# Performance work log

Hardware: AMD Instinct MI355X
Metric: run time of the kernel (lower is better)

## Reference

```python
import jax, jax.numpy as jnp
import numpy as np

GCN_DIM, GEO_DIM, HIDDEN_DIM, TOWER_DIM, RECENT_K = 128, 32, 256, 128, 50
NUM_ITEMS, NUM_USERS = 100000, 16384


def _normalize(x, eps=1e-12):
    # torch F.normalize(dim=1): x / max(||x||, eps)
    n = jnp.linalg.norm(x, axis=1, keepdims=True)
    return x / jnp.maximum(n, eps)


def setup_inputs() -> dict:
    key = jax.random.key(0)
    ks = jax.random.split(key, 16)
    s = 0.05  # weight init scale
    return {
        "item_feat": jax.random.normal(ks[0], (NUM_ITEMS, 2), jnp.float32),
        "gcn_item_emb": jax.random.normal(ks[1], (NUM_ITEMS, GCN_DIM), jnp.float32),
        "gcn_user_emb": jax.random.normal(ks[2], (NUM_USERS, GCN_DIM), jnp.float32),
        "user_items": jax.random.randint(ks[3], (NUM_USERS, RECENT_K), 0, NUM_ITEMS, jnp.int32),
        "Wg": s * jax.random.normal(ks[4], (2, GEO_DIM), jnp.float32),
        "bg": jnp.zeros((GEO_DIM,), jnp.float32),
        "Wi1": s * jax.random.normal(ks[5], (GCN_DIM + GEO_DIM, HIDDEN_DIM), jnp.float32),
        "bi1": jnp.zeros((HIDDEN_DIM,), jnp.float32),
        "Wi2": s * jax.random.normal(ks[6], (HIDDEN_DIM, TOWER_DIM), jnp.float32),
        "bi2": jnp.zeros((TOWER_DIM,), jnp.float32),
        "Wq": s * jax.random.normal(ks[7], (GCN_DIM, TOWER_DIM), jnp.float32),
        "bq": jnp.zeros((TOWER_DIM,), jnp.float32),
        "Wk": s * jax.random.normal(ks[8], (TOWER_DIM, TOWER_DIM), jnp.float32),
        "bk": jnp.zeros((TOWER_DIM,), jnp.float32),
        "Wu1": s * jax.random.normal(ks[9], (GCN_DIM + TOWER_DIM, HIDDEN_DIM), jnp.float32),
        "bu1": jnp.zeros((HIDDEN_DIM,), jnp.float32),
        "Wu2": s * jax.random.normal(ks[10], (HIDDEN_DIM, TOWER_DIM), jnp.float32),
        "bu2": jnp.zeros((TOWER_DIM,), jnp.float32),
    }


def reference(item_feat, gcn_item_emb, gcn_user_emb, user_items,
              Wg, bg, Wi1, bi1, Wi2, bi2, Wq, bq, Wk, bk, Wu1, bu1, Wu2, bu2):
    # ---- encode_items ----
    geo = jax.nn.relu(item_feat @ Wg + bg)                       # [I, GEO]
    xi = jnp.concatenate([geo, gcn_item_emb], axis=1)            # [I, GEO+GCN]
    item_emb = _normalize(jax.nn.relu(xi @ Wi1 + bi1) @ Wi2 + bi2)  # [I, T]

    # ---- encode_users (batched ragged attention pooling) ----
    h = item_emb[user_items]                                     # [U, K, T] gather
    q = gcn_user_emb @ Wq + bq                                   # [U, T]
    k = h @ Wk + bk                                              # [U, K, T]
    scores = jnp.einsum('ut,ukt->uk', q, k)                      # [U, K]
    alpha = jax.nn.softmax(scores, axis=1)                       # softmax over history
    rep = jnp.einsum('uk,ukt->ut', alpha, h)                     # [U, T]
    fused = jnp.concatenate([gcn_user_emb, rep], axis=1)         # [U, GCN+T]
    user_emb = _normalize(jax.nn.relu(fused @ Wu1 + bu1) @ Wu2 + bu2)  # [U, T]

    return jnp.concatenate([item_emb, user_emb], axis=0)         # [I+U, T]
```

## Files before the change

### kernel.cpp

```cpp
#include <hip/hip_runtime.h>
#include <hip/hip_bf16.h>
#include <math.h>

#define NITEMS 100000
#define NUSERS 16384
#define GCN 128
#define GEO 32
#define HIDD 256
#define TD 128
#define RK 50

typedef unsigned int uint;
typedef unsigned short ushort;
typedef __bf16 bf16x8 __attribute__((ext_vector_type(8)));
typedef float f32x4 __attribute__((ext_vector_type(4)));

__device__ __forceinline__ ushort bfb(float x) {
  union { __hip_bfloat16 b; ushort u; } t; t.b = __float2bfloat16(x); return t.u;
}
__device__ __forceinline__ uint packbf2(float a, float b) {
  return (uint)bfb(a) | ((uint)bfb(b) << 16);
}
__device__ __forceinline__ float bflo(uint d) { return __uint_as_float(d << 16); }
__device__ __forceinline__ float bfhi(uint d) { return __uint_as_float(d & 0xffff0000u); }

union U4B { uint4 u; bf16x8 b; };
__device__ __forceinline__ bf16x8 ldfrag(const ushort* p) { U4B t; t.u = *(const uint4*)p; return t.b; }

__global__ __launch_bounds__(256) void prep_convert(
    const float* __restrict__ Wi1, const float* __restrict__ Wi2,
    const float* __restrict__ Wu1, const float* __restrict__ Wu2,
    ushort* __restrict__ Wi1P, ushort* __restrict__ Wi2P,
    ushort* __restrict__ Wu1P, ushort* __restrict__ Wu2P)
{
  int id = blockIdx.x * 256 + threadIdx.x;
  if (id < 40960) {
    int k = id >> 8, c = id & 255;
    Wi1P[(k >> 5) * 8192 + c * 32 + (k & 31)] = bfb(Wi1[id]);
  } else if (id < 73728) {
    int i = id - 40960; int k = i >> 7, c = i & 127;
    Wi2P[(k >> 5) * 4096 + c * 32 + (k & 31)] = bfb(Wi2[i]);
  } else if (id < 139264) {
    int i = id - 73728; int k = i >> 8, c = i & 255;
    Wu1P[(k >> 5) * 8192 + c * 32 + (k & 31)] = bfb(Wu1[i]);
  } else if (id < 172032) {
    int i = id - 139264; int k = i >> 7, c = i & 127;
    Wu2P[(k >> 5) * 4096 + c * 32 + (k & 31)] = bfb(Wu2[i]);
  }
}

__global__ __launch_bounds__(256) void prep_wqk(
    const float* __restrict__ Wq, const float* __restrict__ Wk,
    const float* __restrict__ bq, float* __restrict__ WqkS, float* __restrict__ bqk)
{
  int id = blockIdx.x * 256 + threadIdx.x;
  if (id < 16384) {
    int g = id >> 7, s = id & 127;
    float acc = 0.f;
    for (int t = 0; t < 128; t += 4) {
      float4 a = *(const float4*)(Wq + g * 128 + t);
      float4 b = *(const float4*)(Wk + s * 128 + t);
      acc += a.x * b.x + a.y * b.y + a.z * b.z + a.w * b.w;
    }
    WqkS[g * 128 + s] = acc;
  } else if (id < 16512) {
    int s = id - 16384;
    float acc = 0.f;
    for (int t = 0; t < 128; t += 4) {
      float4 a = *(const float4*)(bq + t);
      float4 b = *(const float4*)(Wk + s * 128 + t);
      acc += a.x * b.x + a.y * b.y + a.z * b.z + a.w * b.w;
    }
    bqk[s] = acc;
  }
}

template <int ROWS, int K1, bool ITEM>
__global__ __launch_bounds__(256, 3) void mlp_kernel(
    const float* __restrict__ xmain,
    const float* __restrict__ feat,
    const float* __restrict__ Wg, const float* __restrict__ bg,
    const ushort* __restrict__ repB,
    const ushort* __restrict__ W1P, const float* __restrict__ b1,
    const ushort* __restrict__ W2P, const float* __restrict__ b2,
    float* __restrict__ outp, ushort* __restrict__ outb, int M)
{
  constexpr int RF = ROWS / 16;
  constexpr int K1CH = K1 / 32;
  constexpr int ASTR = ITEM ? 168 : 264;
  __shared__ __align__(16) ushort s_a[ROWS * 264];
  __shared__ float s_red[ROWS * 4];
  __shared__ float s_inv[ROWS];

  const int tid = threadIdx.x;
  const int wid = tid >> 6, lane = tid & 63, g = lane >> 4, q = lane & 15;
  const int i0 = blockIdx.x * ROWS;

  const ushort* bbase1 = W1P + (wid * 64 + q) * 32 + g * 8;
  bf16x8 bcur[4];
  #pragma unroll
  for (int cf = 0; cf < 4; ++cf) bcur[cf] = ldfrag(bbase1 + cf * 512);

  if constexpr (ITEM) {
    #pragma unroll
    for (int r = 0; r < ROWS / 8; ++r) {
      int lin = r * 256 + tid;
      int it = lin >> 5, c4 = (lin & 31) * 4;
      int row = i0 + it;
      float4 v = make_float4(0.f, 0.f, 0.f, 0.f);
      if (row < M) v = *(const float4*)(xmain + (size_t)row * GCN + c4);
      *(uint*)(&s_a[it * ASTR + GEO + c4])     = packbf2(v.x, v.y);
      *(uint*)(&s_a[it * ASTR + GEO + c4 + 2]) = packbf2(v.z, v.w);
    }
    #pragma unroll
    for (int r = 0; r < ROWS / 8; ++r) {
      int lin = r * 256 + tid;
      int it = lin >> 5, gg = lin & 31;
      int row = i0 + it;
      float f0 = 0.f, f1 = 0.f;
      if (row < M) { f0 = feat[(size_t)row * 2]; f1 = feat[(size_t)row * 2 + 1]; }
      s_a[it * ASTR + gg] = bfb(fmaxf(fmaf(f0, Wg[gg], fmaf(f1, Wg[GEO + gg], bg[gg])), 0.f));
    }
  } else {
    #pragma unroll
    for (int r = 0; r < ROWS / 8; ++r) {
      int lin = r * 256 + tid;
      int it = lin >> 5, c4 = (lin & 31) * 4;
      float4 v = *(const float4*)(xmain + (size_t)(i0 + it) * GCN + c4);
      *(uint*)(&s_a[it * ASTR + c4])     = packbf2(v.x, v.y);
      *(uint*)(&s_a[it * ASTR + c4 + 2]) = packbf2(v.z, v.w);
    }
    #pragma unroll
    for (int r = 0; r < ROWS / 16; ++r) {
      int lin = r * 256 + tid;
      int it = lin >> 4, c8 = (lin & 15) * 8;
      *(uint4*)(&s_a[it * ASTR + GCN + c8]) = *(const uint4*)(repB + (size_t)(i0 + it) * TD + c8);
    }
  }
  __syncthreads();

  f32x4 acc[RF][4];
  #pragma unroll
  for (int cf = 0; cf < 4; ++cf) {
    float bv = b1[wid * 64 + cf * 16 + q];
    f32x4 t = {bv, bv, bv, bv};
    #pragma unroll
    for (int rf = 0; rf < RF; ++rf) acc[rf][cf] = t;
  }
  #pragma unroll
  for (int kb = 0; kb < K1CH; ++kb) {
    bf16x8 bnxt[4];
    if (kb + 1 < K1CH) {
      #pragma unroll
      for (int cf = 0; cf < 4; ++cf) bnxt[cf] = ldfrag(bbase1 + (kb + 1) * 8192 + cf * 512);
    }
    bf16x8 af[RF];
    #pragma unroll
    for (int rf = 0; rf < RF; ++rf) af[rf] = ldfrag(&s_a[(16 * rf + q) * ASTR + kb * 32 + g * 8]);
    #pragma unroll
    for (int rf = 0; rf < RF; ++rf)
      #pragma unroll
      for (int cf = 0; cf < 4; ++cf)
        acc[rf][cf] = __builtin_amdgcn_mfma_f32_16x16x32_bf16(af[rf], bcur[cf], acc[rf][cf], 0, 0, 0);
    if (kb + 1 < K1CH) {
      #pragma unroll
      for (int cf = 0; cf < 4; ++cf) bcur[cf] = bnxt[cf];
    }
  }

  const ushort* bbase2 = W2P + (wid * 32 + q) * 32 + g * 8;
  bf16x8 b2cur[2];
  #pragma unroll
  for (int cf = 0; cf < 2; ++cf) b2cur[cf] = ldfrag(bbase2 + cf * 512);

  __syncthreads();

  #pragma unroll
  for (int rf = 0; rf < RF; ++rf)
    #pragma unroll
    for (int cf = 0; cf < 4; ++cf)
      #pragma unroll
      for (int e = 0; e < 4; ++e)
        s_a[(16 * rf + 4 * g + e) * 264 + wid * 64 + cf * 16 + q] = bfb(fmaxf(acc[rf][cf][e], 0.f));
  __syncthreads();

  f32x4 acc2[RF][2];
  #pragma unroll
  for (int cf = 0; cf < 2; ++cf) {
    float bv = b2[wid * 32 + cf * 16 + q];
    f32x4 t = {bv, bv, bv, bv};
    #pragma unroll
    for (int rf = 0; rf < RF; ++rf) acc2[rf][cf] = t;
  }
  #pragma unroll
  for (int kb = 0; kb < 8; ++kb) {
    bf16x8 bnxt[2];
    if (kb < 7) {
      #pragma unroll
      for (int cf = 0; cf < 2; ++cf) bnxt[cf] = ldfrag(bbase2 + (kb + 1) * 4096 + cf * 512);
    }
    bf16x8 af[RF];
    #pragma unroll
    for (int rf = 0; rf < RF; ++rf) af[rf] = ldfrag(&s_a[(16 * rf + q) * 264 + kb * 32 + g * 8]);
    #pragma unroll
    for (int rf = 0; rf < RF; ++rf)
      #pragma unroll
      for (int cf = 0; cf < 2; ++cf)
        acc2[rf][cf] = __builtin_amdgcn_mfma_f32_16x16x32_bf16(af[rf], b2cur[cf], acc2[rf][cf], 0, 0, 0);
    if (kb < 7) {
      #pragma unroll
      for (int cf = 0; cf < 2; ++cf) b2cur[cf] = bnxt[cf];
    }
  }

  #pragma unroll
  for (int rf = 0; rf < RF; ++rf) {
    #pragma unroll
    for (int e = 0; e < 4; ++e) {
      float p = acc2[rf][0][e] * acc2[rf][0][e] + acc2[rf][1][e] * acc2[rf][1][e];
      p += __shfl_xor(p, 1, 16); p += __shfl_xor(p, 2, 16);
      p += __shfl_xor(p, 4, 16); p += __shfl_xor(p, 8, 16);
      if (q == 0) s_red[(16 * rf + 4 * g + e) * 4 + wid] = p;
    }
  }
  __syncthreads();
  if (tid < ROWS) {
    float s = s_red[tid * 4] + s_red[tid * 4 + 1] + s_red[tid * 4 + 2] + s_red[tid * 4 + 3];
    s_inv[tid] = 1.f / fmaxf(sqrtf(s), 1e-12f);
  }
  __syncthreads();

  #pragma unroll
  for (int rf = 0; rf < RF; ++rf) {
    #pragma unroll
    for (int e = 0; e < 4; ++e) {
      int row = 16 * rf + 4 * g + e;
      int grow = i0 + row;
      if (grow < M) {
        float sc = s_inv[row];
        #pragma unroll
        for (int cf = 0; cf < 2; ++cf) {
          float v = acc2[rf][cf][e] * sc;
          outp[(size_t)grow * TD + wid * 32 + cf * 16 + q] = v;
          if constexpr (ITEM) outb[(size_t)grow * TD + wid * 32 + cf * 16 + q] = bfb(v);
        }
      }
    }
  }
}

__global__ __launch_bounds__(256) void qt_kernel(
    const float* __restrict__ gcn_user, const float* __restrict__ WqkS,
    const float* __restrict__ bqk, float* __restrict__ qt)
{
  __shared__ float s_gue[16 * 132];
  const int tid = threadIdx.x;
  const int u0 = blockIdx.x * 16;
  #pragma unroll
  for (int r = 0; r < 8; ++r) {
    int lin = r * 256 + tid;
    int u = lin >> 7, c = lin & 127;
    s_gue[u * 132 + c] = gcn_user[(size_t)(u0 + u) * GCN + c];
  }
  __syncthreads();
  const int ul = tid >> 4, tx = tid & 15, c0 = tx * 8;
  float a[8];
  { float4 b4 = *(const float4*)(bqk + c0); float4 b5 = *(const float4*)(bqk + c0 + 4);
    a[0]=b4.x; a[1]=b4.y; a[2]=b4.z; a[3]=b4.w; a[4]=b5.x; a[5]=b5.y; a[6]=b5.z; a[7]=b5.w; }
  for (int g = 0; g < 128; ++g) {
    float x = s_gue[ul * 132 + g];
    float4 w4 = *(const float4*)(WqkS + g * 128 + c0);
    float4 w5 = *(const float4*)(WqkS + g * 128 + c0 + 4);
    a[0] = fmaf(x, w4.x, a[0]); a[1] = fmaf(x, w4.y, a[1]);
    a[2] = fmaf(x, w4.z, a[2]); a[3] = fmaf(x, w4.w, a[3]);
    a[4] = fmaf(x, w5.x, a[4]); a[5] = fmaf(x, w5.y, a[5]);
    a[6] = fmaf(x, w5.z, a[6]); a[7] = fmaf(x, w5.w, a[7]);
  }
  float* op = qt + (size_t)(u0 + ul) * TD + c0;
  *(float4*)op = make_float4(a[0], a[1], a[2], a[3]);
  *(float4*)(op + 4) = make_float4(a[4], a[5], a[6], a[7]);
}

__global__ __launch_bounds__(256) void attn_kernel(
    const int* __restrict__ user_items, const float* __restrict__ qt,
    const ushort* __restrict__ itemB, ushort* __restrict__ repB)
{
  __shared__ int s_idx[4][52];
  const int tid = threadIdx.x;
  const int wid = tid >> 6, lane = tid & 63, g = lane >> 4, q = lane & 15;
  const int u = blockIdx.x * 4 + wid;
  const int c0 = q * 8;

  if (lane < 52) s_idx[wid][lane] = (lane < 50) ? user_items[(size_t)u * RK + lane] : 0;
  float qv[8];
  { float4 a = *(const float4*)(qt + (size_t)u * TD + c0);
    float4 b = *(const float4*)(qt + (size_t)u * TD + c0 + 4);
    qv[0]=a.x; qv[1]=a.y; qv[2]=a.z; qv[3]=a.w; qv[4]=b.x; qv[5]=b.y; qv[6]=b.z; qv[7]=b.w; }

  uint4 h[13]; float sc[13];
  #pragma unroll
  for (int i = 0; i < 13; ++i) {
    int j = 4 * i + g;
    int idx = s_idx[wid][j];
    h[i] = *(const uint4*)(itemB + (size_t)idx * TD + c0);
    float p = bflo(h[i].x) * qv[0] + bfhi(h[i].x) * qv[1]
            + bflo(h[i].y) * qv[2] + bfhi(h[i].y) * qv[3]
            + bflo(h[i].z) * qv[4] + bfhi(h[i].z) * qv[5]
            + bflo(h[i].w) * qv[6] + bfhi(h[i].w) * qv[7];
    p += __shfl_xor(p, 1, 16); p += __shfl_xor(p, 2, 16);
    p += __shfl_xor(p, 4, 16); p += __shfl_xor(p, 8, 16);
    sc[i] = (j < RK) ? p : -3.0e38f;
  }
  float m = sc[0];
  #pragma unroll
  for (int i = 1; i < 13; ++i) m = fmaxf(m, sc[i]);
  m = fmaxf(m, __shfl_xor(m, 16, 64));
  m = fmaxf(m, __shfl_xor(m, 32, 64));
  float ssum = 0.f;
  #pragma unroll
  for (int i = 0; i < 13; ++i) { sc[i] = __expf(sc[i] - m); ssum += sc[i]; }
  ssum += __shfl_xor(ssum, 16, 64);
  ssum += __shfl_xor(ssum, 32, 64);
  const float inv = 1.f / ssum;
  float rep[8] = {0, 0, 0, 0, 0, 0, 0, 0};
  #pragma unroll
  for (int i = 0; i < 13; ++i) {
    float a = sc[i] * inv;
    rep[0] = fmaf(a, bflo(h[i].x), rep[0]); rep[1] = fmaf(a, bfhi(h[i].x), rep[1]);
    rep[2] = fmaf(a, bflo(h[i].y), rep[2]); rep[3] = fmaf(a, bfhi(h[i].y), rep[3]);
    rep[4] = fmaf(a, bflo(h[i].z), rep[4]); rep[5] = fmaf(a, bfhi(h[i].z), rep[5]);
    rep[6] = fmaf(a, bflo(h[i].w), rep[6]); rep[7] = fmaf(a, bfhi(h[i].w), rep[7]);
  }
  #pragma unroll
  for (int c = 0; c < 8; ++c) {
    rep[c] += __shfl_xor(rep[c], 16, 64);
    rep[c] += __shfl_xor(rep[c], 32, 64);
  }
  if (g == 0) {
    uint4 o;
    o.x = packbf2(rep[0], rep[1]); o.y = packbf2(rep[2], rep[3]);
    o.z = packbf2(rep[4], rep[5]); o.w = packbf2(rep[6], rep[7]);
    *(uint4*)(repB + (size_t)u * TD + c0) = o;
  }
}

extern "C" void kernel_launch(void* const* d_in, const int* in_sizes, int n_in,
                              void* d_out, int out_size, void* d_ws, size_t ws_size,
                              hipStream_t stream) {
  const float* item_feat  = (const float*)d_in[0];
  const float* gcn_item   = (const float*)d_in[1];
  const float* gcn_user   = (const float*)d_in[2];
  const int*   user_items = (const int*)  d_in[3];
  const float* Wg  = (const float*)d_in[4];
  const float* bg  = (const float*)d_in[5];
  const float* Wi1 = (const float*)d_in[6];
  const float* bi1 = (const float*)d_in[7];
  const float* Wi2 = (const float*)d_in[8];
  const float* bi2 = (const float*)d_in[9];
  const float* Wq  = (const float*)d_in[10];
  const float* bq  = (const float*)d_in[11];
  const float* Wk  = (const float*)d_in[12];
  const float* Wu1 = (const float*)d_in[14];
  const float* bu1 = (const float*)d_in[15];
  const float* Wu2 = (const float*)d_in[16];
  const float* bu2 = (const float*)d_in[17];
  float* out = (float*)d_out;

  char* ws = (char*)d_ws;
  ushort* Wi1P  = (ushort*)(ws + 0);
  ushort* Wi2P  = (ushort*)(ws + 81920);
  ushort* Wu1P  = (ushort*)(ws + 147456);
  ushort* Wu2P  = (ushort*)(ws + 278528);
  float*  WqkS  = (float*) (ws + 344064);
  float*  bqk   = (float*) (ws + 409600);
  float*  qtb   = (float*) (ws + 410112);
  ushort* itemB = (ushort*)(ws + 8798720);
  ushort* repB  = (ushort*)(ws + 34398720);

  prep_convert<<<672, 256, 0, stream>>>(Wi1, Wi2, Wu1, Wu2, Wi1P, Wi2P, Wu1P, Wu2P);
  prep_wqk<<<65, 256, 0, stream>>>(Wq, Wk, bq, WqkS, bqk);
  qt_kernel<<<NUSERS / 16, 256, 0, stream>>>(gcn_user, WqkS, bqk, qtb);
  mlp_kernel<64, 160, true><<<(NITEMS + 63) / 64, 256, 0, stream>>>(
      gcn_item, item_feat, Wg, bg, nullptr, Wi1P, bi1, Wi2P, bi2, out, itemB, NITEMS);
  attn_kernel<<<NUSERS / 4, 256, 0, stream>>>(user_items, qtb, itemB, repB);
  mlp_kernel<32, 256, false><<<NUSERS / 32, 256, 0, stream>>>(
      gcn_user, nullptr, Wg, bg, repB, Wu1P, bu1, Wu2P, bu2, out + (size_t)NITEMS * TD, nullptr, NUSERS);
}
```

Measured before the change: 137.6 us.

## Load MLP input fragments directly from global memory, skipping LDS staging

The MLP kernel no longer stages input rows in shared memory. Each wave builds its MFMA A-fragments straight from global memory, converting fp32 to bf16 in registers and computing the geo features inline. This removes one LDS round trip and a barrier. The item tile shrinks from 64 to 32 rows with occupancy raised to 4 blocks, bounds checks are dropped because 100000 divides by 32, and the two prep kernels are merged into one launch. The trade-offs are redundant global reads across the four waves (each wave loads the same A rows) and the loss of the B-fragment prefetch.

```diff
diff --git a/kernel.cpp b/kernel.cpp
--- a/kernel.cpp
+++ b/kernel.cpp
@@ -26,12 +26,21 @@
 
 union U4B { uint4 u; bf16x8 b; };
 __device__ __forceinline__ bf16x8 ldfrag(const ushort* p) { U4B t; t.u = *(const uint4*)p; return t.b; }
-
-__global__ __launch_bounds__(256) void prep_convert(
+__device__ __forceinline__ bf16x8 pack8(float4 a0, float4 a1) {
+  U4B t;
+  t.u.x = packbf2(a0.x, a0.y); t.u.y = packbf2(a0.z, a0.w);
+  t.u.z = packbf2(a1.x, a1.y); t.u.w = packbf2(a1.z, a1.w);
+  return t.b;
+}
+
+__global__ __launch_bounds__(256) void prep_all(
     const float* __restrict__ Wi1, const float* __restrict__ Wi2,
     const float* __restrict__ Wu1, const float* __restrict__ Wu2,
+    const float* __restrict__ Wq, const float* __restrict__ Wk,
+    const float* __restrict__ bq,
     ushort* __restrict__ Wi1P, ushort* __restrict__ Wi2P,
-    ushort* __restrict__ Wu1P, ushort* __restrict__ Wu2P)
+    ushort* __restrict__ Wu1P, ushort* __restrict__ Wu2P,
+    float* __restrict__ WqkS, float* __restrict__ bqk)
 {
   int id = blockIdx.x * 256 + threadIdx.x;
   if (id < 40960) {
@@ -46,16 +55,8 @@
   } else if (id < 172032) {
     int i = id - 139264; int k = i >> 7, c = i & 127;
     Wu2P[(k >> 5) * 4096 + c * 32 + (k & 31)] = bfb(Wu2[i]);
-  }
-}
-
-__global__ __launch_bounds__(256) void prep_wqk(
-    const float* __restrict__ Wq, const float* __restrict__ Wk,
-    const float* __restrict__ bq, float* __restrict__ WqkS, float* __restrict__ bqk)
-{
-  int id = blockIdx.x * 256 + threadIdx.x;
-  if (id < 16384) {
-    int g = id >> 7, s = id & 127;
+  } else if (id < 188416) {
+    int i = id - 172032; int g = i >> 7, s = i & 127;
     float acc = 0.f;
     for (int t = 0; t < 128; t += 4) {
       float4 a = *(const float4*)(Wq + g * 128 + t);
@@ -63,8 +64,8 @@
       acc += a.x * b.x + a.y * b.y + a.z * b.z + a.w * b.w;
     }
     WqkS[g * 128 + s] = acc;
-  } else if (id < 16512) {
-    int s = id - 16384;
+  } else if (id < 188544) {
+    int s = id - 188416;
     float acc = 0.f;
     for (int t = 0; t < 128; t += 4) {
       float4 a = *(const float4*)(bq + t);
@@ -76,19 +77,18 @@
 }
 
 template <int ROWS, int K1, bool ITEM>
-__global__ __launch_bounds__(256, 3) void mlp_kernel(
+__global__ __launch_bounds__(256, 4) void mlp_kernel(
     const float* __restrict__ xmain,
     const float* __restrict__ feat,
     const float* __restrict__ Wg, const float* __restrict__ bg,
     const ushort* __restrict__ repB,
     const ushort* __restrict__ W1P, const float* __restrict__ b1,
     const ushort* __restrict__ W2P, const float* __restrict__ b2,
-    float* __restrict__ outp, ushort* __restrict__ outb, int M)
+    float* __restrict__ outp, ushort* __restrict__ outb)
 {
   constexpr int RF = ROWS / 16;
   constexpr int K1CH = K1 / 32;
-  constexpr int ASTR = ITEM ? 168 : 264;
-  __shared__ __align__(16) ushort s_a[ROWS * 264];
+  __shared__ __align__(16) ushort s_h[ROWS * 264];
   __shared__ float s_red[ROWS * 4];
   __shared__ float s_inv[ROWS];
 
@@ -96,49 +96,6 @@
   const int wid = tid >> 6, lane = tid & 63, g = lane >> 4, q = lane & 15;
   const int i0 = blockIdx.x * ROWS;
 
-  const ushort* bbase1 = W1P + (wid * 64 + q) * 32 + g * 8;
-  bf16x8 bcur[4];
-  #pragma unroll
-  for (int cf = 0; cf < 4; ++cf) bcur[cf] = ldfrag(bbase1 + cf * 512);
-
-  if constexpr (ITEM) {
-    #pragma unroll
-    for (int r = 0; r < ROWS / 8; ++r) {
-      int lin = r * 256 + tid;
-      int it = lin >> 5, c4 = (lin & 31) * 4;
-      int row = i0 + it;
-      float4 v = make_float4(0.f, 0.f, 0.f, 0.f);
-      if (row < M) v = *(const float4*)(xmain + (size_t)row * GCN + c4);
-      *(uint*)(&s_a[it * ASTR + GEO + c4])     = packbf2(v.x, v.y);
-      *(uint*)(&s_a[it * ASTR + GEO + c4 + 2]) = packbf2(v.z, v.w);
-    }
-    #pragma unroll
-    for (int r = 0; r < ROWS / 8; ++r) {
-      int lin = r * 256 + tid;
-      int it = lin >> 5, gg = lin & 31;
-      int row = i0 + it;
-      float f0 = 0.f, f1 = 0.f;
-      if (row < M) { f0 = feat[(size_t)row * 2]; f1 = feat[(size_t)row * 2 + 1]; }
-      s_a[it * ASTR + gg] = bfb(fmaxf(fmaf(f0, Wg[gg], fmaf(f1, Wg[GEO + gg], bg[gg])), 0.f));
-    }
-  } else {
-    #pragma unroll
-    for (int r = 0; r < ROWS / 8; ++r) {
-      int lin = r * 256 + tid;
-      int it = lin >> 5, c4 = (lin & 31) * 4;
-      float4 v = *(const float4*)(xmain + (size_t)(i0 + it) * GCN + c4);
-      *(uint*)(&s_a[it * ASTR + c4])     = packbf2(v.x, v.y);
-      *(uint*)(&s_a[it * ASTR + c4 + 2]) = packbf2(v.z, v.w);
-    }
-    #pragma unroll
-    for (int r = 0; r < ROWS / 16; ++r) {
-      int lin = r * 256 + tid;
-      int it = lin >> 4, c8 = (lin & 15) * 8;
-      *(uint4*)(&s_a[it * ASTR + GCN + c8]) = *(const uint4*)(repB + (size_t)(i0 + it) * TD + c8);
-    }
-  }
-  __syncthreads();
-
   f32x4 acc[RF][4];
   #pragma unroll
   for (int cf = 0; cf < 4; ++cf) {
@@ -147,33 +104,53 @@
     #pragma unroll
     for (int rf = 0; rf < RF; ++rf) acc[rf][cf] = t;
   }
+  const ushort* bbase1 = W1P + (wid * 64 + q) * 32 + g * 8;
+
   #pragma unroll
   for (int kb = 0; kb < K1CH; ++kb) {
-    bf16x8 bnxt[4];
-    if (kb + 1 < K1CH) {
-      #pragma unroll
-      for (int cf = 0; cf < 4; ++cf) bnxt[cf] = ldfrag(bbase1 + (kb + 1) * 8192 + cf * 512);
-    }
-    bf16x8 af[RF];
-    #pragma unroll
-    for (int rf = 0; rf < RF; ++rf) af[rf] = ldfrag(&s_a[(16 * rf + q) * ASTR + kb * 32 + g * 8]);
+    bf16x8 af[RF], bfr[4];
+    if (ITEM && kb == 0) {
+      float4 w0a = *(const float4*)(Wg + g * 8),      w0b = *(const float4*)(Wg + g * 8 + 4);
+      float4 w1a = *(const float4*)(Wg + 32 + g * 8), w1b = *(const float4*)(Wg + 32 + g * 8 + 4);
+      float4 ba  = *(const float4*)(bg + g * 8),      bb = *(const float4*)(bg + g * 8 + 4);
+      #pragma unroll
+      for (int rf = 0; rf < RF; ++rf) {
+        int row = i0 + q + 16 * rf;
+        float2 f = *(const float2*)(feat + 2 * (size_t)row);
+        float4 lo, hi;
+        lo.x = fmaxf(fmaf(f.x, w0a.x, fmaf(f.y, w1a.x, ba.x)), 0.f);
+        lo.y = fmaxf(fmaf(f.x, w0a.y, fmaf(f.y, w1a.y, ba.y)), 0.f);
+        lo.z = fmaxf(fmaf(f.x, w0a.z, fmaf(f.y, w1a.z, ba.z)), 0.f);
+        lo.w = fmaxf(fmaf(f.x, w0a.w, fmaf(f.y, w1a.w, ba.w)), 0.f);
+        hi.x = fmaxf(fmaf(f.x, w0b.x, fmaf(f.y, w1b.x, bb.x)), 0.f);
+        hi.y = fmaxf(fmaf(f.x, w0b.y, fmaf(f.y, w1b.y, bb.y)), 0.f);
+        hi.z = fmaxf(fmaf(f.x, w0b.z, fmaf(f.y, w1b.z, bb.z)), 0.f);
+        hi.w = fmaxf(fmaf(f.x, w0b.w, fmaf(f.y, w1b.w, bb.w)), 0.f);
+        af[rf] = pack8(lo, hi);
+      }
+    } else if (!ITEM && kb >= K1CH - 4) {
+      #pragma unroll
+      for (int rf = 0; rf < RF; ++rf) {
+        U4B t;
+        t.u = *(const uint4*)(repB + (size_t)(i0 + q + 16 * rf) * TD + (kb - (K1CH - 4)) * 32 + g * 8);
+        af[rf] = t.b;
+      }
+    } else {
+      const int col = (ITEM ? (kb - 1) : kb) * 32 + g * 8;
+      #pragma unroll
+      for (int rf = 0; rf < RF; ++rf) {
+        const float* rp = xmain + (size_t)(i0 + q + 16 * rf) * GCN + col;
+        af[rf] = pack8(*(const float4*)rp, *(const float4*)(rp + 4));
+      }
+    }
+    #pragma unroll
+    for (int cf = 0; cf < 4; ++cf) bfr[cf] = ldfrag(bbase1 + kb * 8192 + cf * 512);
     #pragma unroll
     for (int rf = 0; rf < RF; ++rf)
       #pragma unroll
       for (int cf = 0; cf < 4; ++cf)
-        acc[rf][cf] = __builtin_amdgcn_mfma_f32_16x16x32_bf16(af[rf], bcur[cf], acc[rf][cf], 0, 0, 0);
-    if (kb + 1 < K1CH) {
-      #pragma unroll
-      for (int cf = 0; cf < 4; ++cf) bcur[cf] = bnxt[cf];
-    }
-  }
-
-  const ushort* bbase2 = W2P + (wid * 32 + q) * 32 + g * 8;
-  bf16x8 b2cur[2];
-  #pragma unroll
-  for (int cf = 0; cf < 2; ++cf) b2cur[cf] = ldfrag(bbase2 + cf * 512);
-
-  __syncthreads();
+        acc[rf][cf] = __builtin_amdgcn_mfma_f32_16x16x32_bf16(af[rf], bfr[cf], acc[rf][cf], 0, 0, 0);
+  }
 
   #pragma unroll
   for (int rf = 0; rf < RF; ++rf)
@@ -181,7 +158,7 @@
     for (int cf = 0; cf < 4; ++cf)
       #pragma unroll
       for (int e = 0; e < 4; ++e)
-        s_a[(16 * rf + 4 * g + e) * 264 + wid * 64 + cf * 16 + q] = bfb(fmaxf(acc[rf][cf][e], 0.f));
+        s_h[(16 * rf + 4 * g + e) * 264 + wid * 64 + cf * 16 + q] = bfb(fmaxf(acc[rf][cf][e], 0.f));
   __syncthreads();
 
   f32x4 acc2[RF][2];
@@ -192,24 +169,20 @@
     #pragma unroll
     for (int rf = 0; rf < RF; ++rf) acc2[rf][cf] = t;
   }
-  #pragma unroll
-  for (int kb = 0; kb < 8; ++kb) {
-    bf16x8 bnxt[2];
-    if (kb < 7) {
-      #pragma unroll
-      for (int cf = 0; cf < 2; ++cf) bnxt[cf] = ldfrag(bbase2 + (kb + 1) * 4096 + cf * 512);
-    }
-    bf16x8 af[RF];
-    #pragma unroll
-    for (int rf = 0; rf < RF; ++rf) af[rf] = ldfrag(&s_a[(16 * rf + q) * 264 + kb * 32 + g * 8]);
-    #pragma unroll
-    for (int rf = 0; rf < RF; ++rf)
-      #pragma unroll
-      for (int cf = 0; cf < 2; ++cf)
-        acc2[rf][cf] = __builtin_amdgcn_mfma_f32_16x16x32_bf16(af[rf], b2cur[cf], acc2[rf][cf], 0, 0, 0);
-    if (kb < 7) {
-      #pragma unroll
-      for (int cf = 0; cf < 2; ++cf) b2cur[cf] = bnxt[cf];
+  {
+    const ushort* bbase2 = W2P + (wid * 32 + q) * 32 + g * 8;
+    #pragma unroll
+    for (int kb = 0; kb < 8; ++kb) {
+      bf16x8 af[RF], bf2[2];
+      #pragma unroll
+      for (int rf = 0; rf < RF; ++rf) af[rf] = ldfrag(&s_h[(16 * rf + q) * 264 + kb * 32 + g * 8]);
+      #pragma unroll
+      for (int cf = 0; cf < 2; ++cf) bf2[cf] = ldfrag(bbase2 + kb * 4096 + cf * 512);
+      #pragma unroll
+      for (int rf = 0; rf < RF; ++rf)
+        #pragma unroll
+        for (int cf = 0; cf < 2; ++cf)
+          acc2[rf][cf] = __builtin_amdgcn_mfma_f32_16x16x32_bf16(af[rf], bf2[cf], acc2[rf][cf], 0, 0, 0);
     }
   }
 
@@ -236,14 +209,12 @@
     for (int e = 0; e < 4; ++e) {
       int row = 16 * rf + 4 * g + e;
       int grow = i0 + row;
-      if (grow < M) {
-        float sc = s_inv[row];
-        #pragma unroll
-        for (int cf = 0; cf < 2; ++cf) {
-          float v = acc2[rf][cf][e] * sc;
-          outp[(size_t)grow * TD + wid * 32 + cf * 16 + q] = v;
-          if constexpr (ITEM) outb[(size_t)grow * TD + wid * 32 + cf * 16 + q] = bfb(v);
-        }
+      float sc = s_inv[row];
+      #pragma unroll
+      for (int cf = 0; cf < 2; ++cf) {
+        float v = acc2[rf][cf][e] * sc;
+        outp[(size_t)grow * TD + wid * 32 + cf * 16 + q] = v;
+        if constexpr (ITEM) outb[(size_t)grow * TD + wid * 32 + cf * 16 + q] = bfb(v);
       }
     }
   }
@@ -377,12 +348,12 @@
   ushort* itemB = (ushort*)(ws + 8798720);
   ushort* repB  = (ushort*)(ws + 34398720);
 
-  prep_convert<<<672, 256, 0, stream>>>(Wi1, Wi2, Wu1, Wu2, Wi1P, Wi2P, Wu1P, Wu2P);
-  prep_wqk<<<65, 256, 0, stream>>>(Wq, Wk, bq, WqkS, bqk);
+  prep_all<<<737, 256, 0, stream>>>(Wi1, Wi2, Wu1, Wu2, Wq, Wk, bq,
+                                    Wi1P, Wi2P, Wu1P, Wu2P, WqkS, bqk);
   qt_kernel<<<NUSERS / 16, 256, 0, stream>>>(gcn_user, WqkS, bqk, qtb);
-  mlp_kernel<64, 160, true><<<(NITEMS + 63) / 64, 256, 0, stream>>>(
-      gcn_item, item_feat, Wg, bg, nullptr, Wi1P, bi1, Wi2P, bi2, out, itemB, NITEMS);
+  mlp_kernel<32, 160, true><<<NITEMS / 32, 256, 0, stream>>>(
+      gcn_item, item_feat, Wg, bg, nullptr, Wi1P, bi1, Wi2P, bi2, out, itemB);
   attn_kernel<<<NUSERS / 4, 256, 0, stream>>>(user_items, qtb, itemB, repB);
   mlp_kernel<32, 256, false><<<NUSERS / 32, 256, 0, stream>>>(
-      gcn_user, nullptr, Wg, bg, repB, Wu1P, bu1, Wu2P, bu2, out + (size_t)NITEMS * TD, nullptr, NUSERS);
-}
+      gcn_user, nullptr, Wg, bg, repB, Wu1P, bu1, Wu2P, bu2, out + (size_t)NITEMS * TD, nullptr);
+}
```

Measured after the change: 151.9 us. 1.1x slower.
